# Optimization experiments

Measured on AMD Instinct MI355X. Metric: run time of the kernel, lower is better.

The kernel has to match this reference:

```python
import jax, jax.numpy as jnp
import numpy as np

EPS = 1e-6

def _phi(x):
    # ELU + 1: strictly positive feature map
    return jax.nn.elu(x) + 1.0

def setup_inputs() -> dict:
    key = jax.random.key(0)
    kq, kk, kv = jax.random.split(key, 3)
    shape = (2, 2048, 16, 64)  # [B, T, H, D]
    q = jax.random.normal(kq, shape, dtype=jnp.float32)
    k = jax.random.normal(kk, shape, dtype=jnp.float32)
    v = jax.random.normal(kv, shape, dtype=jnp.float32)
    return {"q": q, "k": k, "v": v}

def reference(q, k, v):
    # Causal linear attention via cumulative prefix sums (math identical to the
    # sequential recurrence S_t = S_{t-1} + phi(k_t)^T v_t, z_t = z_{t-1} + phi(k_t)).
    phi_q = _phi(q)                                   # [B,T,H,D]
    phi_k = _phi(k)                                   # [B,T,H,D]
    outer = jnp.einsum('bthd,bthe->bthde', phi_k, v)  # [B,T,H,D,D]
    prefix_S = jnp.cumsum(outer, axis=1)              # causal state prefix
    prefix_z = jnp.cumsum(phi_k, axis=1)              # causal normalizer prefix
    num = jnp.einsum('bthd,bthde->bthe', phi_q, prefix_S)
    den = jnp.einsum('bthd,bthd->bth', phi_q, prefix_z)[..., None] + EPS
    return num / den
```

## Files before the change

### kernel.cpp

```cpp
#include <hip/hip_runtime.h>


#define BQ 2
#define TT 2048
#define HH 16
#define DD 64
#define CC 64
#define NC (TT / CC)
#define BH (BQ * HH)
#define NCH (BH * NC)
#define LDU 72

typedef __attribute__((ext_vector_type(8))) short short8;
typedef __attribute__((ext_vector_type(4))) float f32x4;

__device__ __forceinline__ float phi_f(float x) {
    return x > 0.f ? x + 1.f : __expf(x);
}
__device__ __forceinline__ unsigned short f2bf(float f) {
    unsigned int u = __float_as_uint(f);
    u += 0x7FFFu + ((u >> 16) & 1u);
    return (unsigned short)(u >> 16);
}
__device__ __forceinline__ float bf2f(unsigned short s) {
    return __uint_as_float(((unsigned int)s) << 16);
}

__global__ __launch_bounds__(256, 4) void k_state(const float* __restrict__ K,
                                                  const float* __restrict__ V,
                                                  float* __restrict__ wsS,
                                                  float* __restrict__ wsZ) {
    __shared__ __align__(16) unsigned short Kt[DD][LDU];
    __shared__ __align__(16) unsigned short Vt[DD][LDU];

    const int cid = blockIdx.x;
    const int bh = cid / NC, c = cid % NC;
    const int b = bh / HH, h = bh % HH;
    const int t0 = c * CC;
    const int tid = threadIdx.x;

#pragma unroll
    for (int w = 0; w < 4; ++w) {
        const int idx = tid + (w << 8);
        const int r = idx >> 4, q4 = (idx & 15) << 2;
        const int g = (((b * TT + t0 + r) * HH + h) << 6) + q4;
        const float4 kv = *(const float4*)(K + g);
        Kt[q4 + 0][r] = f2bf(phi_f(kv.x));
        Kt[q4 + 1][r] = f2bf(phi_f(kv.y));
        Kt[q4 + 2][r] = f2bf(phi_f(kv.z));
        Kt[q4 + 3][r] = f2bf(phi_f(kv.w));
        const float4 vv = *(const float4*)(V + g);
        Vt[q4 + 0][r] = f2bf(vv.x);
        Vt[q4 + 1][r] = f2bf(vv.y);
        Vt[q4 + 2][r] = f2bf(vv.z);
        Vt[q4 + 3][r] = f2bf(vv.w);
    }
    __syncthreads();

    const int wid = tid >> 6, lane = tid & 63;
    const int rg = lane >> 4, cl = lane & 15;

    f32x4 zero4 = {0.f, 0.f, 0.f, 0.f};
    f32x4 acc[4] = {zero4, zero4, zero4, zero4};
#pragma unroll
    for (int kk = 0; kk < 2; ++kk) {
        const short8 a = *(const short8*)&Vt[16 * wid + cl][kk * 32 + rg * 8];
#pragma unroll
        for (int nt = 0; nt < 4; ++nt) {
            const short8 bb = *(const short8*)&Kt[16 * nt + cl][kk * 32 + rg * 8];
            acc[nt] = __builtin_amdgcn_mfma_f32_16x16x32_bf16(a, bb, acc[nt], 0, 0, 0);
        }
    }

    if (tid < DD) {
        float s = 0.f;
#pragma unroll
        for (int tb = 0; tb < 8; ++tb) {
            const short8 v = *(const short8*)&Kt[tid][tb * 8];
#pragma unroll
            for (int i = 0; i < 8; ++i) s += bf2f((unsigned short)v[i]);
        }
        wsZ[cid * DD + tid] = s;
    }

    float* S = wsS + (size_t)cid * (DD * DD);
#pragma unroll
    for (int nt = 0; nt < 4; ++nt)
#pragma unroll
        for (int j = 0; j < 4; ++j)
            S[(16 * wid + 4 * rg + j) * DD + 16 * nt + cl] = acc[nt][j];
}

__global__ __launch_bounds__(256) void k_scan(float* __restrict__ wsS,
                                              float* __restrict__ wsZ) {
    const int blk = blockIdx.x, tid = threadIdx.x;
    if (blk < 512) {
        const int bh = blk >> 4;
        const int off = ((blk & 15) << 8) + tid;
        float* p = wsS + (size_t)bh * NC * (DD * DD) + off;
        float run = 0.f;
#pragma unroll
        for (int c = 0; c < NC; ++c) {
            const float d = p[(size_t)c * (DD * DD)];
            p[(size_t)c * (DD * DD)] = run;
            run += d;
        }
    } else {
        const int zi = ((blk - 512) << 8) + tid;
        const int bh = zi >> 6, d = zi & 63;
        float* p = wsZ + bh * NC * DD + d;
        float run = 0.f;
#pragma unroll
        for (int c = 0; c < NC; ++c) {
            const float dv = p[c * DD];
            p[c * DD] = run;
            run += dv;
        }
    }
}

__global__ __launch_bounds__(256, 4) void k_out(const float* __restrict__ Q,
                                                const float* __restrict__ K,
                                                const float* __restrict__ V,
                                                const float* __restrict__ wsS,
                                                const float* __restrict__ wsZ,
                                                float* __restrict__ O) {
    __shared__ __align__(16) unsigned short Qb[CC][LDU];
    __shared__ __align__(16) unsigned short Kb[CC][LDU];
    __shared__ __align__(16) unsigned short Vt[DD][LDU];
    __shared__ __align__(16) unsigned short St[DD][LDU];
    __shared__ float zp[DD];

    const int cid = blockIdx.x;
    const int bh = cid / NC, c = cid % NC;
    const int b = bh / HH, h = bh % HH;
    const int t0 = c * CC;
    const int tid = threadIdx.x;

#pragma unroll
    for (int w = 0; w < 4; ++w) {
        const int idx = tid + (w << 8);
        const int r = idx >> 4, q4 = (idx & 15) << 2;
        const int g = (((b * TT + t0 + r) * HH + h) << 6) + q4;
        float4 qv = *(const float4*)(Q + g);
        ushort4 us;
        us.x = f2bf(phi_f(qv.x)); us.y = f2bf(phi_f(qv.y));
        us.z = f2bf(phi_f(qv.z)); us.w = f2bf(phi_f(qv.w));
        *(ushort4*)&Qb[r][q4] = us;
        float4 kv = *(const float4*)(K + g);
        us.x = f2bf(phi_f(kv.x)); us.y = f2bf(phi_f(kv.y));
        us.z = f2bf(phi_f(kv.z)); us.w = f2bf(phi_f(kv.w));
        *(ushort4*)&Kb[r][q4] = us;
        const float4 vv = *(const float4*)(V + g);
        Vt[q4 + 0][r] = f2bf(vv.x);
        Vt[q4 + 1][r] = f2bf(vv.y);
        Vt[q4 + 2][r] = f2bf(vv.z);
        Vt[q4 + 3][r] = f2bf(vv.w);
        const float4 sv = *(const float4*)(wsS + (size_t)cid * (DD * DD) + r * DD + q4);
        us.x = f2bf(sv.x); us.y = f2bf(sv.y); us.z = f2bf(sv.z); us.w = f2bf(sv.w);
        *(ushort4*)&St[r][q4] = us;
    }
    if (tid < 16) ((float4*)zp)[tid] = ((const float4*)(wsZ + cid * DD))[tid];
    __syncthreads();

    const int wid = tid >> 6, lane = tid & 63;
    const int rg = lane >> 4, cl = lane & 15;
    f32x4 zero4 = {0.f, 0.f, 0.f, 0.f};

    f32x4 sc[4] = {zero4, zero4, zero4, zero4};
#pragma unroll
    for (int kk = 0; kk < 2; ++kk) {
        const short8 a = *(const short8*)&Qb[16 * wid + cl][kk * 32 + rg * 8];
        for (int nt = 0; nt <= wid; ++nt) {
            const short8 bb = *(const short8*)&Kb[16 * nt + cl][kk * 32 + rg * 8];
            sc[nt] = __builtin_amdgcn_mfma_f32_16x16x32_bf16(a, bb, sc[nt], 0, 0, 0);
        }
    }

    float den4[4], dint[4];
    const float4 zq = *(const float4*)&zp[4 * cl];
#pragma unroll
    for (int j = 0; j < 4; ++j) {
        const int qrow = 16 * wid + 4 * rg + j;
        float s = 0.f;
        for (int nt = 0; nt <= wid; ++nt) {
            if (16 * nt + cl > qrow) sc[nt][j] = 0.f;
            s += sc[nt][j];
        }
        den4[j] = s;
        const ushort4 qv = *(const ushort4*)&Qb[qrow][4 * cl];
        dint[j] = bf2f(qv.x) * zq.x + bf2f(qv.y) * zq.y +
                  bf2f(qv.z) * zq.z + bf2f(qv.w) * zq.w;
    }
#pragma unroll
    for (int m = 1; m < 16; m <<= 1)
#pragma unroll
        for (int j = 0; j < 4; ++j) {
            den4[j] += __shfl_xor(den4[j], m, 64);
            dint[j] += __shfl_xor(dint[j], m, 64);
        }

    f32x4 oa[4] = {zero4, zero4, zero4, zero4};
#pragma unroll
    for (int kk = 0; kk < 2; ++kk) {
        const short8 a = *(const short8*)&Qb[16 * wid + cl][kk * 32 + rg * 8];
#pragma unroll
        for (int nt = 0; nt < 4; ++nt) {
            const short8 bb = *(const short8*)&St[16 * nt + cl][kk * 32 + rg * 8];
            oa[nt] = __builtin_amdgcn_mfma_f32_16x16x32_bf16(a, bb, oa[nt], 0, 0, 0);
        }
    }

    __syncthreads();
#pragma unroll
    for (int nt = 0; nt < 4; ++nt)
#pragma unroll
        for (int j = 0; j < 4; ++j)
            Kb[16 * wid + 4 * rg + j][16 * nt + cl] =
                (nt <= wid) ? f2bf(sc[nt][j]) : (unsigned short)0;
    __syncthreads();

    const int kkmax = (wid >= 2) ? 2 : 1;
    for (int kk = 0; kk < kkmax; ++kk) {
        const short8 a = *(const short8*)&Kb[16 * wid + cl][kk * 32 + rg * 8];
#pragma unroll
        for (int nt = 0; nt < 4; ++nt) {
            const short8 bb = *(const short8*)&Vt[16 * nt + cl][kk * 32 + rg * 8];
            oa[nt] = __builtin_amdgcn_mfma_f32_16x16x32_bf16(a, bb, oa[nt], 0, 0, 0);
        }
    }

#pragma unroll
    for (int j = 0; j < 4; ++j) {
        const int qrow = 16 * wid + 4 * rg + j;
        const float inv = 1.0f / (den4[j] + dint[j] + 1e-6f);
        const int gbase = (((b * TT + t0 + qrow) * HH + h) << 6);
#pragma unroll
        for (int nt = 0; nt < 4; ++nt)
            O[gbase + 16 * nt + cl] = oa[nt][j] * inv;
    }
}

extern "C" void kernel_launch(void* const* d_in, const int* in_sizes, int n_in,
                              void* d_out, int out_size, void* d_ws, size_t ws_size,
                              hipStream_t stream) {
    const float* q = (const float*)d_in[0];
    const float* k = (const float*)d_in[1];
    const float* v = (const float*)d_in[2];
    float* out = (float*)d_out;

    float* wsS = (float*)d_ws;
    float* wsZ = wsS + (size_t)NCH * DD * DD;

    k_state<<<NCH, 256, 0, stream>>>(k, v, wsS, wsZ);
    k_scan<<<520, 256, 0, stream>>>(wsS, wsZ);
    k_out<<<NCH, 256, 0, stream>>>(q, k, v, wsS, wsZ, out);
}
```

Baseline: 115.1 us.

## Store per-chunk state in bf16 workspace and batch-load the scan

Per-chunk KV state matrices are now written to the workspace as bf16 rather than fp32, which halves the traffic for the state write, the scan and the output kernel's read. The scan kernel handles two bf16 columns per thread through 32-bit accesses and preloads all chunk values into registers before accumulating. The running prefix is still summed in fp32, but both the per-chunk partials and the prefix are rounded to bf16, which adds extra quantization error compared with rounding only once in the output kernel.

```diff
diff --git a/kernel.cpp b/kernel.cpp
--- a/kernel.cpp
+++ b/kernel.cpp
@@ -28,7 +28,7 @@
 
 __global__ __launch_bounds__(256, 4) void k_state(const float* __restrict__ K,
                                                   const float* __restrict__ V,
-                                                  float* __restrict__ wsS,
+                                                  unsigned short* __restrict__ wsSh,
                                                   float* __restrict__ wsZ) {
     __shared__ __align__(16) unsigned short Kt[DD][LDU];
     __shared__ __align__(16) unsigned short Vt[DD][LDU];
@@ -83,38 +83,46 @@
         wsZ[cid * DD + tid] = s;
     }
 
-    float* S = wsS + (size_t)cid * (DD * DD);
+    unsigned short* S = wsSh + (size_t)cid * (DD * DD);
 #pragma unroll
     for (int nt = 0; nt < 4; ++nt)
 #pragma unroll
         for (int j = 0; j < 4; ++j)
-            S[(16 * wid + 4 * rg + j) * DD + 16 * nt + cl] = acc[nt][j];
-}
-
-__global__ __launch_bounds__(256) void k_scan(float* __restrict__ wsS,
+            S[(16 * wid + 4 * rg + j) * DD + 16 * nt + cl] = f2bf(acc[nt][j]);
+}
+
+__global__ __launch_bounds__(256) void k_scan(unsigned short* __restrict__ wsSh,
                                               float* __restrict__ wsZ) {
     const int blk = blockIdx.x, tid = threadIdx.x;
-    if (blk < 512) {
-        const int bh = blk >> 4;
-        const int off = ((blk & 15) << 8) + tid;
-        float* p = wsS + (size_t)bh * NC * (DD * DD) + off;
+    if (blk < 256) {
+        const int col = (blk << 8) + tid;
+        const int bh = col >> 11;
+        unsigned int* base =
+            (unsigned int*)(wsSh + (size_t)bh * NC * (DD * DD)) + (col & 2047);
+        unsigned int vals[NC];
+#pragma unroll
+        for (int c = 0; c < NC; ++c) vals[c] = base[c * (DD * DD / 2)];
+        float r0 = 0.f, r1 = 0.f;
+#pragma unroll
+        for (int c = 0; c < NC; ++c) {
+            const unsigned int v = vals[c];
+            base[c * (DD * DD / 2)] =
+                (unsigned int)f2bf(r0) | ((unsigned int)f2bf(r1) << 16);
+            r0 += bf2f((unsigned short)(v & 0xffffu));
+            r1 += bf2f((unsigned short)(v >> 16));
+        }
+    } else {
+        const int zi = ((blk - 256) << 8) + tid;
+        const int bh = zi >> 6, d = zi & 63;
+        float* p = wsZ + (size_t)bh * NC * DD + d;
+        float vals[NC];
+#pragma unroll
+        for (int c = 0; c < NC; ++c) vals[c] = p[c * DD];
         float run = 0.f;
 #pragma unroll
         for (int c = 0; c < NC; ++c) {
-            const float d = p[(size_t)c * (DD * DD)];
-            p[(size_t)c * (DD * DD)] = run;
-            run += d;
-        }
-    } else {
-        const int zi = ((blk - 512) << 8) + tid;
-        const int bh = zi >> 6, d = zi & 63;
-        float* p = wsZ + bh * NC * DD + d;
-        float run = 0.f;
-#pragma unroll
-        for (int c = 0; c < NC; ++c) {
-            const float dv = p[c * DD];
             p[c * DD] = run;
-            run += dv;
+            run += vals[c];
         }
     }
 }
@@ -122,7 +130,7 @@
 __global__ __launch_bounds__(256, 4) void k_out(const float* __restrict__ Q,
                                                 const float* __restrict__ K,
                                                 const float* __restrict__ V,
-                                                const float* __restrict__ wsS,
+                                                const unsigned short* __restrict__ wsSh,
                                                 const float* __restrict__ wsZ,
                                                 float* __restrict__ O) {
     __shared__ __align__(16) unsigned short Qb[CC][LDU];
@@ -156,9 +164,8 @@
         Vt[q4 + 1][r] = f2bf(vv.y);
         Vt[q4 + 2][r] = f2bf(vv.z);
         Vt[q4 + 3][r] = f2bf(vv.w);
-        const float4 sv = *(const float4*)(wsS + (size_t)cid * (DD * DD) + r * DD + q4);
-        us.x = f2bf(sv.x); us.y = f2bf(sv.y); us.z = f2bf(sv.z); us.w = f2bf(sv.w);
-        *(ushort4*)&St[r][q4] = us;
+        *(ushort4*)&St[r][q4] =
+            *(const ushort4*)(wsSh + (size_t)cid * (DD * DD) + r * DD + q4);
     }
     if (tid < 16) ((float4*)zp)[tid] = ((const float4*)(wsZ + cid * DD))[tid];
     __syncthreads();
@@ -249,10 +256,10 @@
     const float* v = (const float*)d_in[2];
     float* out = (float*)d_out;
 
-    float* wsS = (float*)d_ws;
-    float* wsZ = wsS + (size_t)NCH * DD * DD;
-
-    k_state<<<NCH, 256, 0, stream>>>(k, v, wsS, wsZ);
-    k_scan<<<520, 256, 0, stream>>>(wsS, wsZ);
-    k_out<<<NCH, 256, 0, stream>>>(q, k, v, wsS, wsZ, out);
-}
+    float* wsZ = (float*)d_ws;
+    unsigned short* wsSh = (unsigned short*)(wsZ + (size_t)NCH * DD);
+
+    k_state<<<NCH, 256, 0, stream>>>(k, v, wsSh, wsZ);
+    k_scan<<<264, 256, 0, stream>>>(wsSh, wsZ);
+    k_out<<<NCH, 256, 0, stream>>>(q, k, v, wsSh, wsZ, out);
+}
```

New measurement: 109.4 us. -5.0%, faster.
